# Kernel optimization log

Hardware: AMD Instinct MI355X
Metric: run time of the kernel (lower is better)

## Reference

```python
import jax, jax.numpy as jnp
import numpy as np

N_HEAD = 16
N_KV_GROUP = 4
WINDOW = 256


def setup_inputs() -> dict:
    key = jax.random.key(0)
    ks = jax.random.split(key, 5)
    B, T, C = 2, 2048, 1024
    KV = C // N_HEAD * N_KV_GROUP  # 256
    s = 0.02
    return {
        "x": jax.random.normal(ks[0], (B, T, C), jnp.float32),
        "Wq": jax.random.normal(ks[1], (C, C), jnp.float32) * s,
        "bq": jnp.zeros((C,), jnp.float32),
        "Wk": jax.random.normal(ks[2], (C, KV), jnp.float32) * s,
        "bk": jnp.zeros((KV,), jnp.float32),
        "Wv": jax.random.normal(ks[3], (C, KV), jnp.float32) * s,
        "bv": jnp.zeros((KV,), jnp.float32),
        "Wo": jax.random.normal(ks[4], (C, C), jnp.float32) * s,
        "bo": jnp.zeros((C,), jnp.float32),
    }


def reference(x, Wq, bq, Wk, bk, Wv, bv, Wo, bo):
    B, T, C = x.shape
    hd = C // N_HEAD  # head dim = 64
    n_rep = N_HEAD // N_KV_GROUP

    q = x @ Wq + bq                      # [B,T,C]
    k = x @ Wk + bk                      # [B,T,KV]
    v = x @ Wv + bv

    q = q.reshape(B, T, N_HEAD, hd).transpose(0, 2, 1, 3)       # [B,H,T,d]
    k = k.reshape(B, T, N_KV_GROUP, hd).transpose(0, 2, 1, 3)   # [B,G,T,d]
    v = v.reshape(B, T, N_KV_GROUP, hd).transpose(0, 2, 1, 3)

    # GQA: repeat_interleave kv heads along head dim
    k_rep = jnp.repeat(k, n_rep, axis=1)                         # [B,H,T,d]
    v_rep = jnp.repeat(v, n_rep, axis=1)

    att = jnp.einsum("bhqd,bhkd->bhqk", q, k_rep) / jnp.sqrt(jnp.float32(hd))

    # causal + sliding window band mask: q position i attends to j in [i-WINDOW, i]
    i = jnp.arange(T)[:, None]
    j = jnp.arange(T)[None, :]
    band = (j <= i) & (j >= i - WINDOW)                           # [T,T]
    att = jnp.where(band[None, None], att, jnp.float32(-jnp.inf))

    att = jax.nn.softmax(att, axis=-1)
    y = jnp.einsum("bhqk,bhkd->bhqd", att, v_rep)                 # [B,H,T,d]
    y = y.transpose(0, 2, 1, 3).reshape(B, T, C)
    return y @ Wo + bo
```

## Files before the change

### kernel.cpp

```cpp
#include <hip/hip_runtime.h>
#include <hip/hip_bf16.h>

#define TT 2048
#define CC 1024
#define KVD 256
#define QKVD 1536

typedef __bf16 bf16x8 __attribute__((ext_vector_type(8)));
typedef float f32x4 __attribute__((ext_vector_type(4)));

__device__ __forceinline__ void gload_lds16(const __hip_bfloat16* g, __hip_bfloat16* l) {
  __builtin_amdgcn_global_load_lds(
      (const __attribute__((address_space(1))) unsigned int*)g,
      (__attribute__((address_space(3))) unsigned int*)l, 16, 0, 0);
}


__global__ __launch_bounds__(256) void k_prep(const float* __restrict__ x,
                                              const float* __restrict__ Wq,
                                              const float* __restrict__ Wk,
                                              const float* __restrict__ Wv,
                                              const float* __restrict__ Wo,
                                              const float* __restrict__ bq,
                                              const float* __restrict__ bk,
                                              const float* __restrict__ bv,
                                              __hip_bfloat16* __restrict__ xbf,
                                              __hip_bfloat16* __restrict__ wqkvT,
                                              __hip_bfloat16* __restrict__ woT,
                                              float* __restrict__ bqkv) {
  const int bxid = blockIdx.x;
  if (bxid < 4096) {
    size_t idx = ((size_t)bxid * 256 + threadIdx.x) * 4;
    float4 v = *(const float4*)(x + idx);
    xbf[idx + 0] = __float2bfloat16(v.x);
    xbf[idx + 1] = __float2bfloat16(v.y);
    xbf[idx + 2] = __float2bfloat16(v.z);
    xbf[idx + 3] = __float2bfloat16(v.w);
    return;
  }
  if (bxid == 4736) {
    for (int i = threadIdx.x; i < 1536; i += 256) {
      float v;
      if (i < 1024)      v = bq[i];
      else if (i < 1280) v = bk[i - 1024];
      else               v = bv[i - 1280];
      bqkv[i] = v;
    }
    return;
  }
  __shared__ float tile[64][65];
  const float* src;
  int ncols, k0, n0;
  __hip_bfloat16* dst;
  if (bxid < 4480) {
    const int idx = bxid - 4096;
    k0 = (idx & 15) * 64;
    n0 = (idx >> 4) * 64;
    dst = wqkvT;
    if (n0 < 1024)      { src = Wq; ncols = 1024; }
    else if (n0 < 1280) { src = Wk - 1024; ncols = 256; }
    else                { src = Wv - 1280; ncols = 256; }
  } else {
    const int idx = bxid - 4480;
    k0 = (idx & 15) * 64;
    n0 = (idx >> 4) * 64;
    dst = woT; src = Wo; ncols = 1024;
  }
  const int rw = threadIdx.x >> 6;
  const int cl = threadIdx.x & 63;
#pragma unroll
  for (int i = 0; i < 16; ++i) {
    const int kr = rw + i * 4;
    tile[kr][cl] = src[(size_t)(k0 + kr) * ncols + n0 + cl];
  }
  __syncthreads();
#pragma unroll
  for (int i = 0; i < 16; ++i) {
    const int nr = rw + i * 4;
    dst[(size_t)(n0 + nr) * 1024 + k0 + cl] = __float2bfloat16(tile[cl][nr]);
  }
}


__global__ __launch_bounds__(512, 4) void k_gemm1(const __hip_bfloat16* __restrict__ A,
                                                  const __hip_bfloat16* __restrict__ BT,
                                                  const float* __restrict__ bias,
                                                  __hip_bfloat16* __restrict__ C,
                                                  __hip_bfloat16* __restrict__ vtg) {
  __shared__ __hip_bfloat16 As[128][64];
  __shared__ __hip_bfloat16 Bs[128][64];

  const int tid  = threadIdx.x;
  const int m0   = blockIdx.y * 128;
  const int n0   = blockIdx.x * 128;
  const int w    = tid >> 6;
  const int lane = tid & 63;
  const int quad = lane >> 4;
  const int l16  = lane & 15;
  const int wm   = (w & 3) * 32;
  const int wn   = (w >> 2) * 64;

  const int dl_r = lane >> 3;
  const int dl_c = (lane & 7) ^ dl_r;

  const __hip_bfloat16* gA = A + (size_t)(m0 + w * 16 + dl_r) * 1024 + dl_c * 8;
  const __hip_bfloat16* gB = BT + (size_t)(n0 + w * 16 + dl_r) * 1024 + dl_c * 8;

  f32x4 acc[2][4] = {};

  for (int kt = 0; kt < 16; ++kt) {
    const int k0 = kt << 6;
    gload_lds16(gA + k0,                    &As[w * 16][0]);
    gload_lds16(gA + k0 + (size_t)8 * 1024, &As[w * 16 + 8][0]);
    gload_lds16(gB + k0,                    &Bs[w * 16][0]);
    gload_lds16(gB + k0 + (size_t)8 * 1024, &Bs[w * 16 + 8][0]);
    __syncthreads();

#pragma unroll
    for (int ks = 0; ks < 2; ++ks) {
      const int cb = (ks << 2) + quad;
      bf16x8 fa[2], fb[4];
#pragma unroll
      for (int i = 0; i < 2; ++i)
        fa[i] = *(const bf16x8*)&As[wm + i * 16 + l16][(cb ^ (l16 & 7)) << 3];
#pragma unroll
      for (int j = 0; j < 4; ++j)
        fb[j] = *(const bf16x8*)&Bs[wn + j * 16 + l16][(cb ^ (l16 & 7)) << 3];
#pragma unroll
      for (int i = 0; i < 2; ++i)
#pragma unroll
        for (int j = 0; j < 4; ++j)
          acc[i][j] = __builtin_amdgcn_mfma_f32_16x16x32_bf16(fa[i], fb[j], acc[i][j], 0, 0, 0);
    }
    __syncthreads();
  }

#pragma unroll
  for (int j = 0; j < 4; ++j) {
    const int gn = n0 + wn + j * 16 + l16;
    const float bias_v = bias[gn];
    if (gn >= 1280) {
      const int dfull = gn - 1280;
      const int gg = dfull >> 6;
      const int dd = dfull & 63;
#pragma unroll
      for (int i = 0; i < 2; ++i) {
        const int gm = m0 + wm + i * 16 + quad * 4;
        const int bb = gm >> 11;
        const int tl = gm & 2047;
        __hip_bfloat16 tmp[4];
#pragma unroll
        for (int r = 0; r < 4; ++r) tmp[r] = __float2bfloat16(acc[i][j][r] + bias_v);
        *(uint2*)(vtg + ((size_t)((bb * 4 + gg) * 64 + dd)) * TT + tl) = *(const uint2*)tmp;
      }
    } else {
#pragma unroll
      for (int i = 0; i < 2; ++i) {
        const int gmb = m0 + wm + i * 16 + quad * 4;
#pragma unroll
        for (int r = 0; r < 4; ++r)
          C[(size_t)(gmb + r) * QKVD + gn] = __float2bfloat16(acc[i][j][r] + bias_v);
      }
    }
  }
}


__global__ __launch_bounds__(256, 4) void k_gemm2(const __hip_bfloat16* __restrict__ A,
                                                  const __hip_bfloat16* __restrict__ BT,
                                                  const float* __restrict__ bias,
                                                  float* __restrict__ C) {
  __shared__ __hip_bfloat16 As[64][64];
  __shared__ __hip_bfloat16 Bs[128][64];

  const int tid  = threadIdx.x;
  const int m0   = blockIdx.y * 64;
  const int n0   = blockIdx.x * 128;
  const int w    = tid >> 6;
  const int lane = tid & 63;
  const int quad = lane >> 4;
  const int l16  = lane & 15;
  const int wm   = (w >> 1) * 32;
  const int wn   = (w & 1) * 64;

  const int dl_r = lane >> 3;
  const int dl_c = (lane & 7) ^ dl_r;

  const __hip_bfloat16* gA = A + (size_t)(m0 + w * 16 + dl_r) * 1024 + dl_c * 8;
  const __hip_bfloat16* gB = BT + (size_t)(n0 + w * 32 + dl_r) * 1024 + dl_c * 8;

  f32x4 acc[2][4] = {};

  for (int kt = 0; kt < 16; ++kt) {
    const int k0 = kt << 6;
    gload_lds16(gA + k0,                     &As[w * 16][0]);
    gload_lds16(gA + k0 + (size_t)8 * 1024,  &As[w * 16 + 8][0]);
    gload_lds16(gB + k0,                     &Bs[w * 32][0]);
    gload_lds16(gB + k0 + (size_t)8 * 1024,  &Bs[w * 32 + 8][0]);
    gload_lds16(gB + k0 + (size_t)16 * 1024, &Bs[w * 32 + 16][0]);
    gload_lds16(gB + k0 + (size_t)24 * 1024, &Bs[w * 32 + 24][0]);
    __syncthreads();

#pragma unroll
    for (int ks = 0; ks < 2; ++ks) {
      const int cb = (ks << 2) + quad;
      bf16x8 fa[2], fb[4];
#pragma unroll
      for (int i = 0; i < 2; ++i)
        fa[i] = *(const bf16x8*)&As[wm + i * 16 + l16][(cb ^ (l16 & 7)) << 3];
#pragma unroll
      for (int j = 0; j < 4; ++j)
        fb[j] = *(const bf16x8*)&Bs[wn + j * 16 + l16][(cb ^ (l16 & 7)) << 3];
#pragma unroll
      for (int i = 0; i < 2; ++i)
#pragma unroll
        for (int j = 0; j < 4; ++j)
          acc[i][j] = __builtin_amdgcn_mfma_f32_16x16x32_bf16(fa[i], fb[j], acc[i][j], 0, 0, 0);
    }
    __syncthreads();
  }

#pragma unroll
  for (int j = 0; j < 4; ++j) {
    const int gn = n0 + wn + j * 16 + l16;
    const float bias_v = bias[gn];
#pragma unroll
    for (int i = 0; i < 2; ++i) {
      const int gmb = m0 + wm + i * 16 + quad * 4;
#pragma unroll
      for (int r = 0; r < 4; ++r)
        C[(size_t)(gmb + r) * CC + gn] = acc[i][j][r] + bias_v;
    }
  }
}


__global__ __launch_bounds__(256) void k_attn(const __hip_bfloat16* __restrict__ qkv,
                                              const __hip_bfloat16* __restrict__ vtg,
                                              __hip_bfloat16* __restrict__ y) {
  __shared__ __hip_bfloat16 Kb[2][64][64];
  __shared__ __hip_bfloat16 Vb[2][64][64];
  __shared__ __hip_bfloat16 Ps[4][16][72];

  const int t    = threadIdx.x;
  const int w    = t >> 6;
  const int lane = t & 63;
  const int quad = lane >> 4;
  const int l16  = lane & 15;
  const int bx   = blockIdx.x;
  const int h    = blockIdx.y;
  const int b    = blockIdx.z;
  const int g    = h >> 2;
  const int i0   = bx * 64;
  const int qrow      = i0 + w * 16 + l16;
  const int my_q_base = i0 + w * 16 + quad * 4;

  const int lrow = lane >> 3;
  const int cgl  = (lane & 7) ^ lrow;

  const __hip_bfloat16* kg =
      qkv + ((size_t)(b * TT + w * 16 + lrow)) * QKVD + 1024 + g * 64 + cgl * 8;
  const __hip_bfloat16* vg =
      vtg + ((size_t)((b * 4 + g) * 64 + w * 16 + lrow)) * TT + cgl * 8;

  bf16x8 fq[2];
  {
    const __hip_bfloat16* qp = qkv + ((size_t)(b * TT + qrow)) * QKVD + h * 64 + quad * 8;
    fq[0] = *(const bf16x8*)qp;
    fq[1] = *(const bf16x8*)(qp + 32);
  }

  float l_r[4] = {0.f, 0.f, 0.f, 0.f};
  f32x4 o_acc[4] = {};
  const float EC = 0.125f * 1.44269504f;

  const int c_lo = bx >= 4 ? bx - 4 : 0;

  {
    const size_t ko = (size_t)(c_lo * 64) * QKVD;
    gload_lds16(kg + ko,                    &Kb[0][w * 16][0]);
    gload_lds16(kg + ko + (size_t)8 * QKVD, &Kb[0][w * 16 + 8][0]);
    const int vo = c_lo * 64;
    gload_lds16(vg + vo,                  &Vb[0][w * 16][0]);
    gload_lds16(vg + vo + (size_t)8 * TT, &Vb[0][w * 16 + 8][0]);
  }

  int buf = 0;
  for (int c = c_lo; c <= bx; ++c) {
    __syncthreads();
    if (c < bx) {
      const size_t ko = (size_t)((c + 1) * 64) * QKVD;
      gload_lds16(kg + ko,                    &Kb[buf ^ 1][w * 16][0]);
      gload_lds16(kg + ko + (size_t)8 * QKVD, &Kb[buf ^ 1][w * 16 + 8][0]);
      const int vo = (c + 1) * 64;
      gload_lds16(vg + vo,                  &Vb[buf ^ 1][w * 16][0]);
      gload_lds16(vg + vo + (size_t)8 * TT, &Vb[buf ^ 1][w * 16 + 8][0]);
    }

    const int jc = c * 64;

    f32x4 sacc[4] = {};
#pragma unroll
    for (int ks = 0; ks < 2; ++ks) {
      const int sw = (((ks << 2) + quad) ^ (l16 & 7)) << 3;
#pragma unroll
      for (int nt = 0; nt < 4; ++nt) {
        const bf16x8 fk = *(const bf16x8*)&Kb[buf][nt * 16 + l16][sw];
        sacc[nt] = __builtin_amdgcn_mfma_f32_16x16x32_bf16(fq[ks], fk, sacc[nt], 0, 0, 0);
      }
    }

    if (c == bx) {
#pragma unroll
      for (int r = 0; r < 4; ++r) {
        const int gi = my_q_base + r;
#pragma unroll
        for (int nt = 0; nt < 4; ++nt) {
          const int key = jc + nt * 16 + l16;
          const float p = (key <= gi) ? exp2f(sacc[nt][r] * EC) : 0.f;
          l_r[r] += p;
          Ps[w][quad * 4 + r][nt * 16 + l16] = __float2bfloat16(p);
        }
      }
    } else if (bx >= 4 && c == c_lo) {
#pragma unroll
      for (int r = 0; r < 4; ++r) {
        const int glo = my_q_base + r - 256;
#pragma unroll
        for (int nt = 0; nt < 4; ++nt) {
          const int key = jc + nt * 16 + l16;
          const float p = (key >= glo) ? exp2f(sacc[nt][r] * EC) : 0.f;
          l_r[r] += p;
          Ps[w][quad * 4 + r][nt * 16 + l16] = __float2bfloat16(p);
        }
      }
    } else {
#pragma unroll
      for (int r = 0; r < 4; ++r)
#pragma unroll
        for (int nt = 0; nt < 4; ++nt) {
          const float p = exp2f(sacc[nt][r] * EC);
          l_r[r] += p;
          Ps[w][quad * 4 + r][nt * 16 + l16] = __float2bfloat16(p);
        }
    }

    const bf16x8 fp0 = *(const bf16x8*)&Ps[w][l16][quad * 8];
    const bf16x8 fp1 = *(const bf16x8*)&Ps[w][l16][32 + quad * 8];

#pragma unroll
    for (int ks = 0; ks < 2; ++ks) {
      const int sw = (((ks << 2) + quad) ^ (l16 & 7)) << 3;
#pragma unroll
      for (int jt = 0; jt < 4; ++jt) {
        const bf16x8 fv = *(const bf16x8*)&Vb[buf][jt * 16 + l16][sw];
        o_acc[jt] = __builtin_amdgcn_mfma_f32_16x16x32_bf16(ks == 0 ? fp0 : fp1, fv,
                                                            o_acc[jt], 0, 0, 0);
      }
    }
    buf ^= 1;
  }

#pragma unroll
  for (int r = 0; r < 4; ++r) {
#pragma unroll
    for (int d = 1; d < 16; d <<= 1) l_r[r] += __shfl_xor(l_r[r], d);
    const float inv = 1.f / l_r[r];
    __hip_bfloat16* yp = y + ((size_t)(b * TT + my_q_base + r)) * CC + h * 64 + l16;
#pragma unroll
    for (int jt = 0; jt < 4; ++jt)
      yp[jt * 16] = __float2bfloat16(o_acc[jt][r] * inv);
  }
}


extern "C" void kernel_launch(void* const* d_in, const int* in_sizes, int n_in,
                              void* d_out, int out_size, void* d_ws, size_t ws_size,
                              hipStream_t stream) {
  const float* x  = (const float*)d_in[0];
  const float* Wq = (const float*)d_in[1];
  const float* bq = (const float*)d_in[2];
  const float* Wk = (const float*)d_in[3];
  const float* bk = (const float*)d_in[4];
  const float* Wv = (const float*)d_in[5];
  const float* bv = (const float*)d_in[6];
  const float* Wo = (const float*)d_in[7];
  const float* bo = (const float*)d_in[8];
  float* out = (float*)d_out;

  char* ws = (char*)d_ws;
  const size_t M = 2 * TT;
  __hip_bfloat16* xbf   = (__hip_bfloat16*)(ws);
  __hip_bfloat16* qkv   = (__hip_bfloat16*)(ws + 8388608);
  __hip_bfloat16* ybf   = (__hip_bfloat16*)(ws + 20971520);
  __hip_bfloat16* wqkvT = (__hip_bfloat16*)(ws + 29360128);
  __hip_bfloat16* woT   = (__hip_bfloat16*)(ws + 32505856);
  float*          bqkv  = (float*)(ws + 34603008);
  __hip_bfloat16* vtg   = (__hip_bfloat16*)(ws + 34609152);

  k_prep<<<4737, 256, 0, stream>>>(x, Wq, Wk, Wv, Wo, bq, bk, bv,
                                   xbf, wqkvT, woT, bqkv);

  k_gemm1<<<dim3(QKVD / 128, M / 128), 512, 0, stream>>>(xbf, wqkvT, bqkv, qkv, vtg);

  k_attn<<<dim3(TT / 64, 16, 2), 256, 0, stream>>>(qkv, vtg, ybf);

  k_gemm2<<<dim3(CC / 128, M / 64), 256, 0, stream>>>(ybf, woT, bo, out);
}
```

Baseline: 145.1 us.

## Process 128 queries per attention block to share K/V tiles across two wave groups

The attention kernel now uses 512 threads covering 128 query rows, with two groups of four waves that each handle 64 queries. Both groups share a single stream of six K/V chunks loaded into LDS, and each group only computes on the five chunks inside its window. This is meant to cut redundant K/V global loads and the number of blocks. In exchange each group sits idle for one chunk, the grid has fewer and larger blocks, and waves go through more barriers per block.

```diff
diff --git a/kernel.cpp b/kernel.cpp
--- a/kernel.cpp
+++ b/kernel.cpp
@@ -235,12 +235,12 @@
 }
 
 
-__global__ __launch_bounds__(256) void k_attn(const __hip_bfloat16* __restrict__ qkv,
+__global__ __launch_bounds__(512) void k_attn(const __hip_bfloat16* __restrict__ qkv,
                                               const __hip_bfloat16* __restrict__ vtg,
                                               __hip_bfloat16* __restrict__ y) {
   __shared__ __hip_bfloat16 Kb[2][64][64];
   __shared__ __hip_bfloat16 Vb[2][64][64];
-  __shared__ __hip_bfloat16 Ps[4][16][72];
+  __shared__ __hip_bfloat16 Ps[8][16][72];
 
   const int t    = threadIdx.x;
   const int w    = t >> 6;
@@ -251,17 +251,19 @@
   const int h    = blockIdx.y;
   const int b    = blockIdx.z;
   const int g    = h >> 2;
-  const int i0   = bx * 64;
-  const int qrow      = i0 + w * 16 + l16;
-  const int my_q_base = i0 + w * 16 + quad * 4;
+  const int i0   = bx * 128;
+  const int wg   = w >> 2;
+  const int myq0 = i0 + w * 16;
+  const int qrow      = myq0 + l16;
+  const int my_q_base = myq0 + quad * 4;
 
   const int lrow = lane >> 3;
   const int cgl  = (lane & 7) ^ lrow;
 
   const __hip_bfloat16* kg =
-      qkv + ((size_t)(b * TT + w * 16 + lrow)) * QKVD + 1024 + g * 64 + cgl * 8;
+      qkv + ((size_t)(b * TT + w * 8 + lrow)) * QKVD + 1024 + g * 64 + cgl * 8;
   const __hip_bfloat16* vg =
-      vtg + ((size_t)((b * 4 + g) * 64 + w * 16 + lrow)) * TT + cgl * 8;
+      vtg + ((size_t)((b * 4 + g) * 64 + w * 8 + lrow)) * TT + cgl * 8;
 
   bf16x8 fq[2];
   {
@@ -274,88 +276,85 @@
   f32x4 o_acc[4] = {};
   const float EC = 0.125f * 1.44269504f;
 
-  const int c_lo = bx >= 4 ? bx - 4 : 0;
+  const int cc_lo = bx >= 2 ? 0 : (4 - 2 * bx);
+  const int jbase = i0 - 256;
 
   {
-    const size_t ko = (size_t)(c_lo * 64) * QKVD;
-    gload_lds16(kg + ko,                    &Kb[0][w * 16][0]);
-    gload_lds16(kg + ko + (size_t)8 * QKVD, &Kb[0][w * 16 + 8][0]);
-    const int vo = c_lo * 64;
-    gload_lds16(vg + vo,                  &Vb[0][w * 16][0]);
-    gload_lds16(vg + vo + (size_t)8 * TT, &Vb[0][w * 16 + 8][0]);
+    const int jc = jbase + cc_lo * 64;
+    gload_lds16(kg + (size_t)jc * QKVD, &Kb[0][w * 8][0]);
+    gload_lds16(vg + jc,                &Vb[0][w * 8][0]);
   }
 
   int buf = 0;
-  for (int c = c_lo; c <= bx; ++c) {
+  for (int cc = cc_lo; cc < 6; ++cc) {
     __syncthreads();
-    if (c < bx) {
-      const size_t ko = (size_t)((c + 1) * 64) * QKVD;
-      gload_lds16(kg + ko,                    &Kb[buf ^ 1][w * 16][0]);
-      gload_lds16(kg + ko + (size_t)8 * QKVD, &Kb[buf ^ 1][w * 16 + 8][0]);
-      const int vo = (c + 1) * 64;
-      gload_lds16(vg + vo,                  &Vb[buf ^ 1][w * 16][0]);
-      gload_lds16(vg + vo + (size_t)8 * TT, &Vb[buf ^ 1][w * 16 + 8][0]);
-    }
-
-    const int jc = c * 64;
-
-    f32x4 sacc[4] = {};
-#pragma unroll
-    for (int ks = 0; ks < 2; ++ks) {
-      const int sw = (((ks << 2) + quad) ^ (l16 & 7)) << 3;
-#pragma unroll
-      for (int nt = 0; nt < 4; ++nt) {
-        const bf16x8 fk = *(const bf16x8*)&Kb[buf][nt * 16 + l16][sw];
-        sacc[nt] = __builtin_amdgcn_mfma_f32_16x16x32_bf16(fq[ks], fk, sacc[nt], 0, 0, 0);
-      }
-    }
-
-    if (c == bx) {
-#pragma unroll
-      for (int r = 0; r < 4; ++r) {
-        const int gi = my_q_base + r;
+    if (cc < 5) {
+      const int jn = jbase + (cc + 1) * 64;
+      gload_lds16(kg + (size_t)jn * QKVD, &Kb[buf ^ 1][w * 8][0]);
+      gload_lds16(vg + jn,                &Vb[buf ^ 1][w * 8][0]);
+    }
+
+    if (cc >= wg && cc <= 4 + wg) {
+      const int jc = jbase + cc * 64;
+
+      f32x4 sacc[4] = {};
+#pragma unroll
+      for (int ks = 0; ks < 2; ++ks) {
+        const int sw = (((ks << 2) + quad) ^ (l16 & 7)) << 3;
 #pragma unroll
         for (int nt = 0; nt < 4; ++nt) {
-          const int key = jc + nt * 16 + l16;
-          const float p = (key <= gi) ? exp2f(sacc[nt][r] * EC) : 0.f;
-          l_r[r] += p;
-          Ps[w][quad * 4 + r][nt * 16 + l16] = __float2bfloat16(p);
+          const bf16x8 fk = *(const bf16x8*)&Kb[buf][nt * 16 + l16][sw];
+          sacc[nt] = __builtin_amdgcn_mfma_f32_16x16x32_bf16(fq[ks], fk, sacc[nt], 0, 0, 0);
         }
       }
-    } else if (bx >= 4 && c == c_lo) {
-#pragma unroll
-      for (int r = 0; r < 4; ++r) {
-        const int glo = my_q_base + r - 256;
-#pragma unroll
-        for (int nt = 0; nt < 4; ++nt) {
-          const int key = jc + nt * 16 + l16;
-          const float p = (key >= glo) ? exp2f(sacc[nt][r] * EC) : 0.f;
-          l_r[r] += p;
-          Ps[w][quad * 4 + r][nt * 16 + l16] = __float2bfloat16(p);
+
+      if (cc == 4 + wg) {
+#pragma unroll
+        for (int r = 0; r < 4; ++r) {
+          const int gi = my_q_base + r;
+#pragma unroll
+          for (int nt = 0; nt < 4; ++nt) {
+            const int key = jc + nt * 16 + l16;
+            const float p = (key <= gi) ? exp2f(sacc[nt][r] * EC) : 0.f;
+            l_r[r] += p;
+            Ps[w][quad * 4 + r][nt * 16 + l16] = __float2bfloat16(p);
+          }
         }
+      } else if (cc == wg) {
+#pragma unroll
+        for (int r = 0; r < 4; ++r) {
+          const int glo = my_q_base + r - 256;
+#pragma unroll
+          for (int nt = 0; nt < 4; ++nt) {
+            const int key = jc + nt * 16 + l16;
+            const float p = (key >= glo) ? exp2f(sacc[nt][r] * EC) : 0.f;
+            l_r[r] += p;
+            Ps[w][quad * 4 + r][nt * 16 + l16] = __float2bfloat16(p);
+          }
+        }
+      } else {
+#pragma unroll
+        for (int r = 0; r < 4; ++r)
+#pragma unroll
+          for (int nt = 0; nt < 4; ++nt) {
+            const float p = exp2f(sacc[nt][r] * EC);
+            l_r[r] += p;
+            Ps[w][quad * 4 + r][nt * 16 + l16] = __float2bfloat16(p);
+          }
       }
-    } else {
-#pragma unroll
-      for (int r = 0; r < 4; ++r)
-#pragma unroll
-        for (int nt = 0; nt < 4; ++nt) {
-          const float p = exp2f(sacc[nt][r] * EC);
-          l_r[r] += p;
-          Ps[w][quad * 4 + r][nt * 16 + l16] = __float2bfloat16(p);
+
+      const bf16x8 fp0 = *(const bf16x8*)&Ps[w][l16][quad * 8];
+      const bf16x8 fp1 = *(const bf16x8*)&Ps[w][l16][32 + quad * 8];
+
+#pragma unroll
+      for (int ks = 0; ks < 2; ++ks) {
+        const int sw = (((ks << 2) + quad) ^ (l16 & 7)) << 3;
+#pragma unroll
+        for (int jt = 0; jt < 4; ++jt) {
+          const bf16x8 fv = *(const bf16x8*)&Vb[buf][jt * 16 + l16][sw];
+          o_acc[jt] = __builtin_amdgcn_mfma_f32_16x16x32_bf16(ks == 0 ? fp0 : fp1, fv,
+                                                              o_acc[jt], 0, 0, 0);
         }
-    }
-
-    const bf16x8 fp0 = *(const bf16x8*)&Ps[w][l16][quad * 8];
-    const bf16x8 fp1 = *(const bf16x8*)&Ps[w][l16][32 + quad * 8];
-
-#pragma unroll
-    for (int ks = 0; ks < 2; ++ks) {
-      const int sw = (((ks << 2) + quad) ^ (l16 & 7)) << 3;
-#pragma unroll
-      for (int jt = 0; jt < 4; ++jt) {
-        const bf16x8 fv = *(const bf16x8*)&Vb[buf][jt * 16 + l16][sw];
-        o_acc[jt] = __builtin_amdgcn_mfma_f32_16x16x32_bf16(ks == 0 ? fp0 : fp1, fv,
-                                                            o_acc[jt], 0, 0, 0);
       }
     }
     buf ^= 1;
@@ -403,7 +402,7 @@
 
   k_gemm1<<<dim3(QKVD / 128, M / 128), 512, 0, stream>>>(xbf, wqkvT, bqkv, qkv, vtg);
 
-  k_attn<<<dim3(TT / 64, 16, 2), 256, 0, stream>>>(qkv, vtg, ybf);
+  k_attn<<<dim3(TT / 128, 16, 2), 512, 0, stream>>>(qkv, vtg, ybf);
 
   k_gemm2<<<dim3(CC / 128, M / 64), 256, 0, stream>>>(ybf, woT, bo, out);
 }
```

Result: no change. 142.5 us (-1.8%).
